# Kernel optimization log

Hardware: AMD Instinct MI355X
Metric: run time of the kernel (lower is better)

The kernel has to match this reference:

```python
import jax, jax.numpy as jnp
import numpy as np

NUM_EXPERTS = 8
TOP_K = 2
D_IN = 1024
D_OUT = 1024
N_TOKENS = 8192


def setup_inputs() -> dict:
    key = jax.random.key(0)
    ks = jax.random.split(key, 7)
    s_in = 1.0 / np.sqrt(D_IN)
    s_out = 1.0 / np.sqrt(D_OUT)
    return {
        "x": jax.random.normal(ks[0], (N_TOKENS, D_IN), dtype=jnp.float32),
        # stacked expert params: fc1 [E, D_in, D_out], fc2 [E, D_out, D_out]
        "W1": jax.random.uniform(ks[1], (NUM_EXPERTS, D_IN, D_OUT), jnp.float32, -s_in, s_in),
        "b1": jax.random.uniform(ks[2], (NUM_EXPERTS, D_OUT), jnp.float32, -s_in, s_in),
        "W2": jax.random.uniform(ks[3], (NUM_EXPERTS, D_OUT, D_OUT), jnp.float32, -s_out, s_out),
        "b2": jax.random.uniform(ks[4], (NUM_EXPERTS, D_OUT), jnp.float32, -s_out, s_out),
        "Wg": jax.random.uniform(ks[5], (D_IN, NUM_EXPERTS), jnp.float32, -s_in, s_in),
        "bg": jax.random.uniform(ks[6], (NUM_EXPERTS,), jnp.float32, -s_in, s_in),
    }


def reference(x, W1, b1, W2, b2, Wg, bg):
    n = x.shape[0]
    # gating
    gate_logits = x @ Wg + bg                      # [N, E]
    gate_weights = jax.nn.softmax(gate_logits, axis=1)
    if TOP_K < NUM_EXPERTS:
        topk_vals, topk_idx = jax.lax.top_k(gate_weights, TOP_K)  # [N, K]
        rows = jnp.arange(n)[:, None]
        gate_weights = jnp.zeros_like(gate_weights).at[rows, topk_idx].set(topk_vals)
    # dense all-expert MLP fan-out (faithful to the original wasteful compute)
    h = jax.nn.relu(jnp.einsum('nd,edh->enh', x, W1) + b1[:, None, :])  # [E, N, H]
    y = jnp.einsum('enh,eho->eno', h, W2) + b2[:, None, :]               # [E, N, O]
    # weighted combine over experts
    out = jnp.einsum('ne,eno->no', gate_weights, y)                      # [N, O]
    return out
```

## Files before the change

kernel.cpp:

```cpp
#include <hip/hip_runtime.h>

#define NUM_E 8
#define N_TOK 8192
#define DIM 1024

typedef __attribute__((ext_vector_type(8))) short short8;
typedef __attribute__((ext_vector_type(4))) float f32x4;

__device__ __forceinline__ unsigned short f2bf(float f) {
  unsigned int u = __float_as_uint(f);
  u = (u + 0x7fffu + ((u >> 16) & 1u)) >> 16;
  return (unsigned short)u;
}

__device__ __forceinline__ void async16(const unsigned short* g, unsigned short* l) {
  __builtin_amdgcn_global_load_lds((const __attribute__((address_space(1))) void*)g,
                                   (__attribute__((address_space(3))) void*)l,
                                   16, 0, 0);
}

__device__ __forceinline__ void wtile_transpose(const float* src, unsigned short* dst,
                                                int tk, int tn, float (*s)[65]) {
  const int k0 = tk * 64, n0 = tn * 64;
  const int t = threadIdx.x;
  {
    const int rr = t >> 4;
    const int c4 = (t & 15) * 4;
#pragma unroll
    for (int i = 0; i < 4; ++i) {
      const int k = i * 16 + rr;
      float4 v = *(const float4*)&src[(size_t)(k0 + k) * DIM + n0 + c4];
      s[c4 + 0][k] = v.x; s[c4 + 1][k] = v.y;
      s[c4 + 2][k] = v.z; s[c4 + 3][k] = v.w;
    }
  }
  __syncthreads();
  {
    const int kq = (t & 7) * 8;
    const int nn = t >> 3;
#pragma unroll
    for (int r = 0; r < 2; ++r) {
      const int n = r * 32 + nn;
      union { unsigned short us[8]; uint4 v; } o;
#pragma unroll
      for (int j = 0; j < 8; ++j) o.us[j] = f2bf(s[n][kq + j]);
      *(uint4*)(dst + (size_t)(n0 + n) * DIM + k0 + kq) = o.v;
    }
  }
}

__global__ __launch_bounds__(256) void prep_gate_w1_kernel(
    const float* __restrict__ x, const float* __restrict__ Wg,
    const float* __restrict__ bg, int* __restrict__ tok_top,
    float2* __restrict__ tok_wts, unsigned short* __restrict__ xb,
    float* __restrict__ out,
    const float* __restrict__ W1, unsigned short* __restrict__ W1T) {
  __shared__ float s[64][65];
  const int bid = blockIdx.x;
  if (bid & 1) {
    const int wv = bid >> 1;
    wtile_transpose(W1 + (size_t)(wv >> 8) * (DIM * DIM),
                    W1T + (size_t)(wv >> 8) * (DIM * DIM),
                    (wv >> 4) & 15, wv & 15, s);
    return;
  }
  const int gb = bid >> 1;
  {
    float4* oz = (float4*)(out + (size_t)gb * 4096);
    const float4 z4 = {0.f, 0.f, 0.f, 0.f};
#pragma unroll
    for (int i = 0; i < 4; ++i) oz[i * 256 + threadIdx.x] = z4;
  }
  const int wave = threadIdx.x >> 6;
  const int lane = threadIdx.x & 63;
  const int n = gb * 4 + wave;
  const float4* xr = (const float4*)(x + (size_t)n * DIM);
  unsigned short* xbr = xb + (size_t)n * DIM;
  float acc[NUM_E];
#pragma unroll
  for (int e = 0; e < NUM_E; ++e) acc[e] = 0.f;
#pragma unroll
  for (int it = 0; it < 4; ++it) {
    float4 xv = xr[it * 64 + lane];
    const float4* wr = (const float4*)Wg + (size_t)(it * 256 + lane * 4) * 2;
    float xs[4] = {xv.x, xv.y, xv.z, xv.w};
    union { unsigned short u[4]; uint2 v; } oo;
    oo.u[0] = f2bf(xv.x); oo.u[1] = f2bf(xv.y);
    oo.u[2] = f2bf(xv.z); oo.u[3] = f2bf(xv.w);
    *(uint2*)(xbr + it * 256 + lane * 4) = oo.v;
#pragma unroll
    for (int dd = 0; dd < 4; ++dd) {
      float4 wa = wr[dd * 2 + 0];
      float4 wb = wr[dd * 2 + 1];
      acc[0] += xs[dd] * wa.x; acc[1] += xs[dd] * wa.y;
      acc[2] += xs[dd] * wa.z; acc[3] += xs[dd] * wa.w;
      acc[4] += xs[dd] * wb.x; acc[5] += xs[dd] * wb.y;
      acc[6] += xs[dd] * wb.z; acc[7] += xs[dd] * wb.w;
    }
  }
#pragma unroll
  for (int e = 0; e < NUM_E; ++e)
#pragma unroll
    for (int off = 32; off > 0; off >>= 1)
      acc[e] += __shfl_down(acc[e], off);
  if (lane == 0) {
    float p[NUM_E];
    float mx = -1e30f;
#pragma unroll
    for (int e = 0; e < NUM_E; ++e) { p[e] = acc[e] + bg[e]; mx = fmaxf(mx, p[e]); }
    float ss = 0.f;
#pragma unroll
    for (int e = 0; e < NUM_E; ++e) { p[e] = expf(p[e] - mx); ss += p[e]; }
    float inv = 1.f / ss;
    int i0 = 0;
#pragma unroll
    for (int e = 1; e < NUM_E; ++e) if (p[e] > p[i0]) i0 = e;
    int i1 = (i0 == 0) ? 1 : 0;
#pragma unroll
    for (int e = 0; e < NUM_E; ++e) if (e != i0 && p[e] > p[i1]) i1 = e;
    tok_top[n] = i0 | (i1 << 8);
    tok_wts[n] = make_float2(p[i0] * inv, p[i1] * inv);
  }
}

__global__ __launch_bounds__(256) void gate2_kernel(const int* __restrict__ tok_top,
                                                    const float2* __restrict__ tok_wts,
                                                    int* __restrict__ counts,
                                                    int* __restrict__ tok_idx,
                                                    float* __restrict__ tok_w) {
  __shared__ int wsum[4];
  __shared__ int btot;
  const int e = blockIdx.x;
  const int t = threadIdx.x;
  const int lane = t & 63;
  const int wave = t >> 6;
  unsigned mask = 0;
  int cnt = 0;
#pragma unroll 8
  for (int j = 0; j < 32; ++j) {
    int top = tok_top[t * 32 + j];
    bool m = ((top & 0xff) == e) || (((top >> 8) & 0xff) == e);
    mask |= (unsigned)m << j;
    cnt += m;
  }
  int inc = cnt;
#pragma unroll
  for (int off = 1; off < 64; off <<= 1) {
    int v = __shfl_up(inc, off);
    if (lane >= off) inc += v;
  }
  if (lane == 63) wsum[wave] = inc;
  __syncthreads();
  if (t < 4) {
    int v = wsum[t];
    int ssum = v;
#pragma unroll
    for (int off = 1; off < 4; off <<= 1) {
      int u = __shfl_up(ssum, off);
      if (lane >= off) ssum += u;
    }
    wsum[t] = ssum - v;
    if (t == 3) btot = ssum;
  }
  __syncthreads();
  int slot = wsum[wave] + inc - cnt;
#pragma unroll 8
  for (int j = 0; j < 32; ++j) {
    if ((mask >> j) & 1u) {
      int n = t * 32 + j;
      int top = tok_top[n];
      float2 ww = tok_wts[n];
      bool m0 = (top & 0xff) == e;
      tok_idx[e * N_TOK + slot] = n;
      tok_w[e * N_TOK + slot] = m0 ? ww.x : ww.y;
      slot++;
    }
  }
  if (t == 0) counts[e] = btot;
}

__global__ __launch_bounds__(256, 4) void fc1_w2t_kernel(
    const unsigned short* __restrict__ A_src,
    const unsigned short* __restrict__ wT,
    const float* __restrict__ W2, unsigned short* __restrict__ W2T,
    const float* __restrict__ bias,
    const int* __restrict__ counts,
    const int* __restrict__ tok_idx,
    unsigned short* __restrict__ h_out)
{
  __shared__ __align__(16) unsigned char smem[33792];
  const int bid = blockIdx.x;
  const int role = bid % 3;
  if (role != 0) {
    const int wv = (bid / 3) * 2 + role - 1;
    if (wv < 2048)
      wtile_transpose(W2 + (size_t)(wv >> 8) * (DIM * DIM),
                      W2T + (size_t)(wv >> 8) * (DIM * DIM),
                      (wv >> 4) & 15, wv & 15, (float(*)[65])smem);
    return;
  }
  const int xcd  = bid & 7;
  const int rank = bid / 24;
  const int mt   = xcd * 17 + (rank >> 3);
  const int nt   = rank & 7;

  int e = -1, m0 = 0, base = 0;
  {
    int acc_tiles = 0, acc_rows = 0;
#pragma unroll
    for (int i = 0; i < NUM_E; ++i) {
      int c = counts[i];
      int t = (c + 127) >> 7;
      if (mt >= acc_tiles && mt < acc_tiles + t) {
        e = i; m0 = (mt - acc_tiles) * 128; base = acc_rows;
      }
      acc_tiles += t;
      acc_rows += t * 128;
    }
  }
  if (e < 0) return;
  const int count = counts[e];
  const int n0 = nt * 128;

  const int tid  = threadIdx.x;
  const int wave = tid >> 6;
  const int lane = tid & 63;
  const int l15  = lane & 15;
  const int quad = lane >> 4;
  const int wm   = wave & 1;
  const int wn   = wave >> 1;

  unsigned short* sA = (unsigned short*)smem;
  unsigned short* sB = (unsigned short*)(smem + 16384);

  const int r0 = 32 * wave + l15;
  const int r1 = r0 + 16;
  int s0 = m0 + r0; s0 = s0 < count ? s0 : count - 1;
  int s1 = m0 + r1; s1 = s1 < count ? s1 : count - 1;
  const size_t aOff0 = (size_t)tok_idx[e * N_TOK + s0] * DIM;
  const size_t aOff1 = (size_t)tok_idx[e * N_TOK + s1] * DIM;
  const unsigned short* wte = wT + (size_t)e * DIM * DIM;
  const size_t bOff0 = (size_t)(n0 + r0) * DIM;
  const size_t bOff1 = (size_t)(n0 + r1) * DIM;
  const int kl = quad * 8;
  const int c0 = (2 * wave + 0) * 512;
  const int c1 = (2 * wave + 1) * 512;

  const f32x4 vzero = {0.f, 0.f, 0.f, 0.f};
  f32x4 acc[4][4];
#pragma unroll
  for (int i = 0; i < 4; ++i)
#pragma unroll
    for (int j = 0; j < 4; ++j) acc[i][j] = vzero;

  for (int k0 = 0; k0 < DIM; k0 += 64) {
    async16(A_src + aOff0 + k0 + kl,      &sA[c0]);
    async16(A_src + aOff1 + k0 + kl,      &sA[c1]);
    async16(A_src + aOff0 + k0 + 32 + kl, &sA[4096 + c0]);
    async16(A_src + aOff1 + k0 + 32 + kl, &sA[4096 + c1]);
    async16(wte + bOff0 + k0 + kl,        &sB[c0]);
    async16(wte + bOff1 + k0 + kl,        &sB[c1]);
    async16(wte + bOff0 + k0 + 32 + kl,   &sB[4096 + c0]);
    async16(wte + bOff1 + k0 + 32 + kl,   &sB[4096 + c1]);
    __syncthreads();
#pragma unroll
    for (int s = 0; s < 2; ++s) {
      short8 af[4], bfr[4];
#pragma unroll
      for (int i = 0; i < 4; ++i)
        af[i] = *(const short8*)&sA[s * 4096 + (wm * 4 + i) * 512 + lane * 8];
#pragma unroll
      for (int j = 0; j < 4; ++j)
        bfr[j] = *(const short8*)&sB[s * 4096 + (wn * 4 + j) * 512 + lane * 8];
#pragma unroll
      for (int i = 0; i < 4; ++i)
#pragma unroll
        for (int j = 0; j < 4; ++j)
          acc[i][j] = __builtin_amdgcn_mfma_f32_16x16x32_bf16(af[i], bfr[j], acc[i][j], 0, 0, 0);
    }
    __syncthreads();
  }

  float bv[4];
#pragma unroll
  for (int j = 0; j < 4; ++j)
    bv[j] = bias[e * DIM + n0 + (wn * 4 + j) * 16 + l15];

#pragma unroll
  for (int i = 0; i < 4; ++i) {
    const int rbase = (wm * 4 + i) * 16 + quad * 4;
#pragma unroll
    for (int r = 0; r < 4; ++r) {
      const int slot = m0 + rbase + r;
      if (slot < count) {
        unsigned short* hp = h_out + (size_t)(base + slot) * DIM + n0;
#pragma unroll
        for (int j = 0; j < 4; ++j) {
          float v = acc[i][j][r] + bv[j];
          v = v > 0.f ? v : 0.f;
          hp[(wn * 4 + j) * 16 + l15] = f2bf(v);
        }
      }
    }
  }
}

__global__ __launch_bounds__(256) void fc2_kernel(
    const unsigned short* __restrict__ A_src,
    const unsigned short* __restrict__ wT,
    const float* __restrict__ bias,
    const int* __restrict__ counts,
    const int* __restrict__ tok_idx,
    const float* __restrict__ tok_w,
    float* __restrict__ out)
{
  const int bid = blockIdx.x;
  const int xcd = bid & 7;
  const int mt  = xcd * 33 + (bid >> 6);
  const int nt  = (bid >> 3) & 7;

  int e = -1, m0 = 0, base = 0;
  {
    int at = 0, ar = 0;
#pragma unroll
    for (int i = 0; i < NUM_E; ++i) {
      int c = counts[i];
      int t = (c + 63) >> 6;
      if (mt >= at && mt < at + t) { e = i; m0 = (mt - at) * 64; base = ar; }
      at += t;
      ar += ((c + 127) >> 7) * 128;
    }
  }
  if (e < 0) return;
  const int count = counts[e];
  const int n0 = nt * 128;

  const int tid  = threadIdx.x;
  const int wave = tid >> 6;
  const int lane = tid & 63;
  const int l15  = lane & 15;
  const int quad = lane >> 4;
  const int wm   = wave & 1;
  const int wn   = wave >> 1;

  __shared__ unsigned short sA[4096];
  __shared__ unsigned short sB[8192];

  const size_t aOff  = (size_t)(base + m0 + 16 * wave + l15) * DIM + quad * 8;
  const unsigned short* wte = wT + (size_t)e * DIM * DIM;
  const size_t bOff0 = (size_t)(n0 + 32 * wave + l15) * DIM + quad * 8;
  const size_t bOff1 = bOff0 + 16 * DIM;
  const int cA  = wave * 512;
  const int cB0 = 2 * wave * 512;
  const int cB1 = cB0 + 512;

  const f32x4 vzero = {0.f, 0.f, 0.f, 0.f};
  f32x4 acc[2][4];
#pragma unroll
  for (int i = 0; i < 2; ++i)
#pragma unroll
    for (int j = 0; j < 4; ++j) acc[i][j] = vzero;

  for (int k0 = 0; k0 < DIM; k0 += 64) {
    async16(A_src + aOff + k0,       &sA[cA]);
    async16(A_src + aOff + k0 + 32,  &sA[2048 + cA]);
    async16(wte + bOff0 + k0,        &sB[cB0]);
    async16(wte + bOff1 + k0,        &sB[cB1]);
    async16(wte + bOff0 + k0 + 32,   &sB[4096 + cB0]);
    async16(wte + bOff1 + k0 + 32,   &sB[4096 + cB1]);
    __syncthreads();
#pragma unroll
    for (int s = 0; s < 2; ++s) {
      short8 af[2], bfr[4];
#pragma unroll
      for (int i = 0; i < 2; ++i)
        af[i] = *(const short8*)&sA[s * 2048 + (wm * 2 + i) * 512 + lane * 8];
#pragma unroll
      for (int j = 0; j < 4; ++j)
        bfr[j] = *(const short8*)&sB[s * 4096 + (wn * 4 + j) * 512 + lane * 8];
#pragma unroll
      for (int i = 0; i < 2; ++i)
#pragma unroll
        for (int j = 0; j < 4; ++j)
          acc[i][j] = __builtin_amdgcn_mfma_f32_16x16x32_bf16(af[i], bfr[j], acc[i][j], 0, 0, 0);
    }
    __syncthreads();
  }

  float bv[4];
#pragma unroll
  for (int j = 0; j < 4; ++j)
    bv[j] = bias[e * DIM + n0 + (wn * 4 + j) * 16 + l15];

#pragma unroll
  for (int i = 0; i < 2; ++i) {
    const int rbase = (wm * 2 + i) * 16 + quad * 4;
#pragma unroll
    for (int r = 0; r < 4; ++r) {
      const int slot = m0 + rbase + r;
      if (slot < count) {
        const int tok = tok_idx[e * N_TOK + slot];
        const float wgt = tok_w[e * N_TOK + slot];
        float* op = out + (size_t)tok * DIM + n0;
#pragma unroll
        for (int j = 0; j < 4; ++j) {
          float v = acc[i][j][r] + bv[j];
          atomicAdd(&op[(wn * 4 + j) * 16 + l15], wgt * v);
        }
      }
    }
  }
}


extern "C" void kernel_launch(void* const* d_in, const int* in_sizes, int n_in,
                              void* d_out, int out_size, void* d_ws, size_t ws_size,
                              hipStream_t stream) {
  const float* x  = (const float*)d_in[0];
  const float* W1 = (const float*)d_in[1];
  const float* b1 = (const float*)d_in[2];
  const float* W2 = (const float*)d_in[3];
  const float* b2 = (const float*)d_in[4];
  const float* Wg = (const float*)d_in[5];
  const float* bg = (const float*)d_in[6];
  float* out = (float*)d_out;

  char* ws = (char*)d_ws;
  int*            counts  = (int*)(ws);
  int*            tok_idx = (int*)(ws + 1024);
  float*          tok_w   = (float*)(ws + 263168);
  unsigned short* xb      = (unsigned short*)(ws + 525312);
  unsigned short* w1t     = (unsigned short*)(ws + 525312 + 16777216ull);
  unsigned short* w2t     = (unsigned short*)(ws + 525312 + 2ull * 16777216ull);
  unsigned short* hb      = (unsigned short*)(ws + 525312 + 3ull * 16777216ull);
  size_t gate_off = 525312 + 3ull * 16777216ull + 35651584ull;
  int*            tok_top = (int*)(ws + gate_off);
  float2*         tok_wts = (float2*)(ws + gate_off + 32768);

  prep_gate_w1_kernel<<<4096, 256, 0, stream>>>(x, Wg, bg, tok_top, tok_wts, xb,
                                                out, W1, w1t);
  gate2_kernel<<<8, 256, 0, stream>>>(tok_top, tok_wts, counts, tok_idx, tok_w);
  fc1_w2t_kernel<<<3264, 256, 0, stream>>>(xb, w1t, W2, w2t, b1,
                                           counts, tok_idx, hb);
  fc2_kernel<<<2112, 256, 0, stream>>>(hb, w2t, b2, counts, tok_idx, tok_w, out);
}
```

Baseline: 419.7 us.

## Enlarge fc2 M tile to 128 and move W1 transpose into gate2 launch

fc2 now uses 128x128 output tiles instead of 64x128, so each B fragment feeds twice as many MFMAs and fewer blocks are launched. Token indices and weights are staged in LDS before the atomic epilogue, and launch_bounds asks for 4 blocks per SM. The W1 bf16 transpose moves out of the gating kernel and into the tiny gate2 launch, so the gate2 work is no longer a lone 8-block kernel. This adds register pressure from the larger accumulator and leaves more padded rows per expert.

```diff
diff --git a/kernel.cpp b/kernel.cpp
--- a/kernel.cpp
+++ b/kernel.cpp
@@ -49,31 +49,20 @@
   }
 }
 
-__global__ __launch_bounds__(256) void prep_gate_w1_kernel(
+__global__ __launch_bounds__(256) void prep_gate_kernel(
     const float* __restrict__ x, const float* __restrict__ Wg,
     const float* __restrict__ bg, int* __restrict__ tok_top,
     float2* __restrict__ tok_wts, unsigned short* __restrict__ xb,
-    float* __restrict__ out,
-    const float* __restrict__ W1, unsigned short* __restrict__ W1T) {
-  __shared__ float s[64][65];
-  const int bid = blockIdx.x;
-  if (bid & 1) {
-    const int wv = bid >> 1;
-    wtile_transpose(W1 + (size_t)(wv >> 8) * (DIM * DIM),
-                    W1T + (size_t)(wv >> 8) * (DIM * DIM),
-                    (wv >> 4) & 15, wv & 15, s);
-    return;
-  }
-  const int gb = bid >> 1;
+    float* __restrict__ out) {
   {
-    float4* oz = (float4*)(out + (size_t)gb * 4096);
+    float4* oz = (float4*)(out + (size_t)blockIdx.x * 4096);
     const float4 z4 = {0.f, 0.f, 0.f, 0.f};
 #pragma unroll
     for (int i = 0; i < 4; ++i) oz[i * 256 + threadIdx.x] = z4;
   }
   const int wave = threadIdx.x >> 6;
   const int lane = threadIdx.x & 63;
-  const int n = gb * 4 + wave;
+  const int n = blockIdx.x * 4 + wave;
   const float4* xr = (const float4*)(x + (size_t)n * DIM);
   unsigned short* xbr = xb + (size_t)n * DIM;
   float acc[NUM_E];
@@ -123,14 +112,22 @@
   }
 }
 
-__global__ __launch_bounds__(256) void gate2_kernel(const int* __restrict__ tok_top,
-                                                    const float2* __restrict__ tok_wts,
-                                                    int* __restrict__ counts,
-                                                    int* __restrict__ tok_idx,
-                                                    float* __restrict__ tok_w) {
+__global__ __launch_bounds__(256) void prep_w1_gate2_kernel(
+    const float* __restrict__ W1, unsigned short* __restrict__ W1T,
+    const int* __restrict__ tok_top, const float2* __restrict__ tok_wts,
+    int* __restrict__ counts, int* __restrict__ tok_idx,
+    float* __restrict__ tok_w) {
+  __shared__ float s[64][65];
   __shared__ int wsum[4];
   __shared__ int btot;
-  const int e = blockIdx.x;
+  const int bid = blockIdx.x;
+  if (bid < 2048) {
+    wtile_transpose(W1 + (size_t)(bid >> 8) * (DIM * DIM),
+                    W1T + (size_t)(bid >> 8) * (DIM * DIM),
+                    (bid >> 4) & 15, bid & 15, s);
+    return;
+  }
+  const int e = bid - 2048;
   const int t = threadIdx.x;
   const int lane = t & 63;
   const int wave = t >> 6;
@@ -305,7 +302,7 @@
   }
 }
 
-__global__ __launch_bounds__(256) void fc2_kernel(
+__global__ __launch_bounds__(256, 4) void fc2_kernel(
     const unsigned short* __restrict__ A_src,
     const unsigned short* __restrict__ wT,
     const float* __restrict__ bias,
@@ -316,19 +313,21 @@
 {
   const int bid = blockIdx.x;
   const int xcd = bid & 7;
-  const int mt  = xcd * 33 + (bid >> 6);
+  const int mt  = xcd * 17 + (bid >> 6);
   const int nt  = (bid >> 3) & 7;
 
   int e = -1, m0 = 0, base = 0;
   {
-    int at = 0, ar = 0;
+    int acc_tiles = 0, acc_rows = 0;
 #pragma unroll
     for (int i = 0; i < NUM_E; ++i) {
       int c = counts[i];
-      int t = (c + 63) >> 6;
-      if (mt >= at && mt < at + t) { e = i; m0 = (mt - at) * 64; base = ar; }
-      at += t;
-      ar += ((c + 127) >> 7) * 128;
+      int t = (c + 127) >> 7;
+      if (mt >= acc_tiles && mt < acc_tiles + t) {
+        e = i; m0 = (mt - acc_tiles) * 128; base = acc_rows;
+      }
+      acc_tiles += t;
+      acc_rows += t * 128;
     }
   }
   if (e < 0) return;
@@ -343,43 +342,57 @@
   const int wm   = wave & 1;
   const int wn   = wave >> 1;
 
-  __shared__ unsigned short sA[4096];
-  __shared__ unsigned short sB[8192];
-
-  const size_t aOff  = (size_t)(base + m0 + 16 * wave + l15) * DIM + quad * 8;
+  __shared__ unsigned short sA[2 * 4096];
+  __shared__ unsigned short sB[2 * 4096];
+  __shared__ int   s_tok[128];
+  __shared__ float s_w[128];
+
+  if (tid < 128) {
+    int slot = m0 + tid;
+    int cs = slot < count ? slot : count - 1;
+    s_tok[tid] = tok_idx[e * N_TOK + cs];
+    s_w[tid]   = slot < count ? tok_w[e * N_TOK + slot] : 0.f;
+  }
+
+  const int r0 = 32 * wave + l15;
+  const int r1 = r0 + 16;
+  const size_t aOff0 = (size_t)(base + m0 + r0) * DIM;
+  const size_t aOff1 = (size_t)(base + m0 + r1) * DIM;
   const unsigned short* wte = wT + (size_t)e * DIM * DIM;
-  const size_t bOff0 = (size_t)(n0 + 32 * wave + l15) * DIM + quad * 8;
-  const size_t bOff1 = bOff0 + 16 * DIM;
-  const int cA  = wave * 512;
-  const int cB0 = 2 * wave * 512;
-  const int cB1 = cB0 + 512;
+  const size_t bOff0 = (size_t)(n0 + r0) * DIM;
+  const size_t bOff1 = (size_t)(n0 + r1) * DIM;
+  const int kl = quad * 8;
+  const int c0 = (2 * wave + 0) * 512;
+  const int c1 = (2 * wave + 1) * 512;
 
   const f32x4 vzero = {0.f, 0.f, 0.f, 0.f};
-  f32x4 acc[2][4];
-#pragma unroll
-  for (int i = 0; i < 2; ++i)
+  f32x4 acc[4][4];
+#pragma unroll
+  for (int i = 0; i < 4; ++i)
 #pragma unroll
     for (int j = 0; j < 4; ++j) acc[i][j] = vzero;
 
   for (int k0 = 0; k0 < DIM; k0 += 64) {
-    async16(A_src + aOff + k0,       &sA[cA]);
-    async16(A_src + aOff + k0 + 32,  &sA[2048 + cA]);
-    async16(wte + bOff0 + k0,        &sB[cB0]);
-    async16(wte + bOff1 + k0,        &sB[cB1]);
-    async16(wte + bOff0 + k0 + 32,   &sB[4096 + cB0]);
-    async16(wte + bOff1 + k0 + 32,   &sB[4096 + cB1]);
+    async16(A_src + aOff0 + k0 + kl,      &sA[c0]);
+    async16(A_src + aOff1 + k0 + kl,      &sA[c1]);
+    async16(A_src + aOff0 + k0 + 32 + kl, &sA[4096 + c0]);
+    async16(A_src + aOff1 + k0 + 32 + kl, &sA[4096 + c1]);
+    async16(wte + bOff0 + k0 + kl,        &sB[c0]);
+    async16(wte + bOff1 + k0 + kl,        &sB[c1]);
+    async16(wte + bOff0 + k0 + 32 + kl,   &sB[4096 + c0]);
+    async16(wte + bOff1 + k0 + 32 + kl,   &sB[4096 + c1]);
     __syncthreads();
 #pragma unroll
     for (int s = 0; s < 2; ++s) {
-      short8 af[2], bfr[4];
-#pragma unroll
-      for (int i = 0; i < 2; ++i)
-        af[i] = *(const short8*)&sA[s * 2048 + (wm * 2 + i) * 512 + lane * 8];
+      short8 af[4], bfr[4];
+#pragma unroll
+      for (int i = 0; i < 4; ++i)
+        af[i] = *(const short8*)&sA[s * 4096 + (wm * 4 + i) * 512 + lane * 8];
 #pragma unroll
       for (int j = 0; j < 4; ++j)
         bfr[j] = *(const short8*)&sB[s * 4096 + (wn * 4 + j) * 512 + lane * 8];
 #pragma unroll
-      for (int i = 0; i < 2; ++i)
+      for (int i = 0; i < 4; ++i)
 #pragma unroll
         for (int j = 0; j < 4; ++j)
           acc[i][j] = __builtin_amdgcn_mfma_f32_16x16x32_bf16(af[i], bfr[j], acc[i][j], 0, 0, 0);
@@ -393,19 +406,20 @@
     bv[j] = bias[e * DIM + n0 + (wn * 4 + j) * 16 + l15];
 
 #pragma unroll
-  for (int i = 0; i < 2; ++i) {
-    const int rbase = (wm * 2 + i) * 16 + quad * 4;
+  for (int i = 0; i < 4; ++i) {
+    const int rbase = (wm * 4 + i) * 16 + quad * 4;
 #pragma unroll
     for (int r = 0; r < 4; ++r) {
       const int slot = m0 + rbase + r;
       if (slot < count) {
-        const int tok = tok_idx[e * N_TOK + slot];
-        const float wgt = tok_w[e * N_TOK + slot];
+        const int rl = rbase + r;
+        const int tok = s_tok[rl];
+        const float w = s_w[rl];
         float* op = out + (size_t)tok * DIM + n0;
 #pragma unroll
         for (int j = 0; j < 4; ++j) {
           float v = acc[i][j][r] + bv[j];
-          atomicAdd(&op[(wn * 4 + j) * 16 + l15], wgt * v);
+          atomicAdd(&op[(wn * 4 + j) * 16 + l15], w * v);
         }
       }
     }
@@ -437,10 +451,10 @@
   int*            tok_top = (int*)(ws + gate_off);
   float2*         tok_wts = (float2*)(ws + gate_off + 32768);
 
-  prep_gate_w1_kernel<<<4096, 256, 0, stream>>>(x, Wg, bg, tok_top, tok_wts, xb,
-                                                out, W1, w1t);
-  gate2_kernel<<<8, 256, 0, stream>>>(tok_top, tok_wts, counts, tok_idx, tok_w);
+  prep_gate_kernel<<<2048, 256, 0, stream>>>(x, Wg, bg, tok_top, tok_wts, xb, out);
+  prep_w1_gate2_kernel<<<2056, 256, 0, stream>>>(W1, w1t, tok_top, tok_wts,
+                                                 counts, tok_idx, tok_w);
   fc1_w2t_kernel<<<3264, 256, 0, stream>>>(xb, w1t, W2, w2t, b1,
                                            counts, tok_idx, hb);
-  fc2_kernel<<<2112, 256, 0, stream>>>(hb, w2t, b2, counts, tok_idx, tok_w, out);
-}
+  fc2_kernel<<<1088, 256, 0, stream>>>(hb, w2t, b2, counts, tok_idx, tok_w, out);
+}
```

After: 384.6 us. 1.09x faster.
